# Kernel tuning notes

Measured on AMD Instinct MI355X. Metric: run time of the kernel, lower is better.

Reference implementation:

```python
import jax, jax.numpy as jnp
import numpy as np

EPS = 1e-6  # denominator guard used in LN Killing-ReLU


def ln_linear(W, x):
    # LNLinear: mix feature channels. x: [B,F,K,N], W: [G,F] -> [B,G,K,N]
    return jnp.einsum('gf,bfkn->bgkn', W, x)


def killing_so3(a, b):
    return -2.0 * jnp.sum(a * b, axis=2, keepdims=True)  # [B,F,1,N]


def ln_killing_relu(Wd, x):
    # LNKillingRelu: learned direction d, project out x's component along d
    # when the Killing form is non-negative (equivalent of VN-ReLU).
    d = ln_linear(Wd, x)
    kf = killing_so3(x, d)
    dd = killing_so3(d, d)
    return jnp.where(kf < 0, x, x - (kf / (dd + EPS)) * d)


def _forward(x, t, R, m, w1_lin, w1_dir, w2_lin, w2_dir, wb, wo):
    B = x.shape[0]
    x4 = x[..., None]  # [B,1,3,1]
    # control input u(t) = R @ 10*[sin t, cos t, sin t]
    u = R @ (10.0 * jnp.stack([jnp.sin(t), jnp.cos(t), jnp.sin(t)]))  # [3]
    u = jnp.broadcast_to(u[None, None, :, None], (B, 1, 3, 1))
    xin = jnp.concatenate([x4, u], axis=1)  # [B,2,3,1]

    # equivariant mixing matrices from learned m: [3,20] -> features [1,20,3,1]
    Rm = jnp.transpose(R @ m)[None, :, :, None]  # rearrange 'k f -> 1 f k 1'
    m1 = ln_killing_relu(w1_dir, ln_linear(w1_lin, Rm))  # [1,3,3,1]
    m2 = ln_killing_relu(w2_dir, ln_linear(w2_lin, Rm))
    m1 = jnp.transpose(m1[0, :, :, 0])  # rearrange '1 f k 1 -> k f' -> [3,3]
    m2 = jnp.transpose(m2[0, :, :, 0])
    M1 = m1 @ m1.T  # [3,3]
    M2 = m2 @ m2.T

    # LNLinearAndLieBracketChannelMix (residual_connect=True)
    h = ln_linear(wb, xin)  # [B,20,3,1]
    d1 = jnp.einsum('kl,bfln->bfkn', M1, h)
    d2 = jnp.einsum('kl,bfln->bfkn', M2, h)
    h = jnp.cross(d1, d2, axis=2) + h  # so3 Lie bracket = cross product; residual

    out = ln_linear(wo, h)  # [B,1,3,1]
    return out[..., 0]  # rearrange 'b f d 1 -> b f d'


def setup_inputs():
    key = jax.random.key(0)
    ks = jax.random.split(key, 8)
    B, FM = 1000000, 20
    x = jax.random.normal(ks[0], (B, 1, 3), dtype=jnp.float32)
    t = jnp.array(0.7, dtype=jnp.float32)
    R = jnp.eye(3, dtype=jnp.float32)
    m = 0.1 * jax.random.normal(ks[1], (3, FM), dtype=jnp.float32)
    w1_lin = jax.random.normal(ks[2], (3, FM), dtype=jnp.float32) / np.sqrt(FM)
    w1_dir = jax.random.normal(ks[3], (3, 3), dtype=jnp.float32) / np.sqrt(3.0)
    w2_lin = jax.random.normal(ks[4], (3, FM), dtype=jnp.float32) / np.sqrt(FM)
    w2_dir = jax.random.normal(ks[5], (3, 3), dtype=jnp.float32) / np.sqrt(3.0)
    wb = jax.random.normal(ks[6], (FM, 2), dtype=jnp.float32) / np.sqrt(2.0)
    wo = jax.random.normal(ks[7], (1, FM), dtype=jnp.float32) / np.sqrt(FM)
    return {"x": x, "t": t, "R": R, "m": m, "w1_lin": w1_lin, "w1_dir": w1_dir,
            "w2_lin": w2_lin, "w2_dir": w2_dir, "wb": wb, "wo": wo}


def reference(x, t, R, m, w1_lin, w1_dir, w2_lin, w2_dir, wb, wo):
    return _forward(x, t, R, m, w1_lin, w1_dir, w2_lin, w2_dir, wb, wo)
```

## Files before the change

### kernel.cpp

```cpp
#include <hip/hip_runtime.h>
#include <math.h>

#define LN_EPS 1e-6f


__device__ inline void compute_M(const float* wl , const float* wd ,
                                 const float Rm[20][3], float M[3][3]) {
    float y[3][3];
    for (int g = 0; g < 3; ++g)
        for (int k = 0; k < 3; ++k) {
            float s = 0.f;
            for (int f = 0; f < 20; ++f) s += wl[g * 20 + f] * Rm[f][k];
            y[g][k] = s;
        }
    float d[3][3];
    for (int g = 0; g < 3; ++g)
        for (int k = 0; k < 3; ++k) {
            float s = 0.f;
            for (int f = 0; f < 3; ++f) s += wd[g * 3 + f] * y[f][k];
            d[g][k] = s;
        }
    float mm[3][3];
    for (int f = 0; f < 3; ++f) {
        float kf = -2.f * (y[f][0] * d[f][0] + y[f][1] * d[f][1] + y[f][2] * d[f][2]);
        float dd = -2.f * (d[f][0] * d[f][0] + d[f][1] * d[f][1] + d[f][2] * d[f][2]);
        float coef = kf / (dd + LN_EPS);
        for (int k = 0; k < 3; ++k)
            mm[f][k] = (kf < 0.f) ? y[f][k] : (y[f][k] - coef * d[f][k]);
    }
    for (int k = 0; k < 3; ++k)
        for (int l = 0; l < 3; ++l) {
            float s = 0.f;
            for (int f = 0; f < 3; ++f) s += mm[f][k] * mm[f][l];
            M[k][l] = s;
        }
}

__global__ void setup_kernel(const float* __restrict__ t, const float* __restrict__ R,
                             const float* __restrict__ m, const float* __restrict__ w1l,
                             const float* __restrict__ w1d, const float* __restrict__ w2l,
                             const float* __restrict__ w2d, const float* __restrict__ wb,
                             const float* __restrict__ wo, float* __restrict__ ws) {
    if (threadIdx.x != 0 || blockIdx.x != 0) return;

    const float tt = t[0];
    const float st = sinf(tt), ct = cosf(tt);
    const float uv[3] = {10.f * st, 10.f * ct, 10.f * st};
    float u[3];
    for (int i = 0; i < 3; ++i)
        u[i] = R[i * 3 + 0] * uv[0] + R[i * 3 + 1] * uv[1] + R[i * 3 + 2] * uv[2];

    float Rm[20][3];
    for (int f = 0; f < 20; ++f)
        for (int k = 0; k < 3; ++k) {
            float s = 0.f;
            for (int j = 0; j < 3; ++j) s += R[k * 3 + j] * m[j * 20 + f];
            Rm[f][k] = s;
        }

    float M1[3][3], M2[3][3];
    compute_M(w1l, w1d, Rm, M1);
    compute_M(w2l, w2d, Rm, M2);

    float v1[3], v2[3];
    for (int k = 0; k < 3; ++k) {
        v1[k] = M1[k][0] * u[0] + M1[k][1] * u[1] + M1[k][2] * u[2];
        v2[k] = M2[k][0] * u[0] + M2[k][1] * u[1] + M2[k][2] * u[2];
    }

    float Sa = 0.f, Sb = 0.f, Saa = 0.f, Sab = 0.f, Sbb = 0.f;
    for (int g = 0; g < 20; ++g) {
        float a = wb[g * 2 + 0], b = wb[g * 2 + 1], w = wo[g];
        Sa += w * a; Sb += w * b;
        Saa += w * a * a; Sab += w * a * b; Sbb += w * b * b;
    }

    auto hat = [](const float v[3], float H[3][3]) {
        H[0][0] = 0.f;    H[0][1] = -v[2]; H[0][2] = v[1];
        H[1][0] = v[2];   H[1][1] = 0.f;   H[1][2] = -v[0];
        H[2][0] = -v[1];  H[2][1] = v[0];  H[2][2] = 0.f;
    };
    float H1[3][3], H2[3][3];
    hat(v1, H1);
    hat(v2, H2);

    float A[3][3];
    for (int i = 0; i < 3; ++i)
        for (int j = 0; j < 3; ++j) {
            float s = 0.f;
            for (int k = 0; k < 3; ++k)
                s += -H2[i][k] * M1[k][j] + H1[i][k] * M2[k][j];
            A[i][j] = Sab * s + ((i == j) ? Sa : 0.f);
        }

    float cr[3] = {v1[1] * v2[2] - v1[2] * v2[1],
                   v1[2] * v2[0] - v1[0] * v2[2],
                   v1[0] * v2[1] - v1[1] * v2[0]};
    float c0[3];
    for (int k = 0; k < 3; ++k) c0[k] = Sbb * cr[k] + Sb * u[k];

    for (int i = 0; i < 9; ++i) ws[i] = M1[i / 3][i % 3];
    for (int i = 0; i < 9; ++i) ws[9 + i] = M2[i / 3][i % 3];
    for (int i = 0; i < 9; ++i) ws[18 + i] = A[i / 3][i % 3];
    for (int k = 0; k < 3; ++k) ws[27 + k] = c0[k];
    ws[30] = Saa;
}


__device__ inline void point_op(const float* c, float X, float Y, float Z,
                                float& o0, float& o1, float& o2) {
    float p0 = c[0] * X + c[1] * Y + c[2] * Z;
    float p1 = c[3] * X + c[4] * Y + c[5] * Z;
    float p2 = c[6] * X + c[7] * Y + c[8] * Z;
    float q0 = c[9] * X + c[10] * Y + c[11] * Z;
    float q1 = c[12] * X + c[13] * Y + c[14] * Z;
    float q2 = c[15] * X + c[16] * Y + c[17] * Z;
    float cr0 = p1 * q2 - p2 * q1;
    float cr1 = p2 * q0 - p0 * q2;
    float cr2 = p0 * q1 - p1 * q0;
    float S = c[30];
    o0 = S * cr0 + c[18] * X + c[19] * Y + c[20] * Z + c[27];
    o1 = S * cr1 + c[21] * X + c[22] * Y + c[23] * Z + c[28];
    o2 = S * cr2 + c[24] * X + c[25] * Y + c[26] * Z + c[29];
}

__global__ __launch_bounds__(256) void main_kernel(const float* __restrict__ x,
                                                   float* __restrict__ out,
                                                   const float* __restrict__ ws,
                                                   int n4, int tail) {
    __shared__ float c[31];
    if (threadIdx.x < 31) c[threadIdx.x] = ws[threadIdx.x];
    __syncthreads();

    int tid = blockIdx.x * blockDim.x + threadIdx.x;

    if (tid < n4) {
        const float4* xin = (const float4*)x;
        float4 a = xin[tid * 3 + 0];
        float4 b = xin[tid * 3 + 1];
        float4 d = xin[tid * 3 + 2];
        float xs[12] = {a.x, a.y, a.z, a.w, b.x, b.y, b.z, b.w, d.x, d.y, d.z, d.w};
        float os[12];
#pragma unroll
        for (int p = 0; p < 4; ++p)
            point_op(c, xs[p * 3 + 0], xs[p * 3 + 1], xs[p * 3 + 2],
                     os[p * 3 + 0], os[p * 3 + 1], os[p * 3 + 2]);
        float4* op = (float4*)out;
        op[tid * 3 + 0] = make_float4(os[0], os[1], os[2], os[3]);
        op[tid * 3 + 1] = make_float4(os[4], os[5], os[6], os[7]);
        op[tid * 3 + 2] = make_float4(os[8], os[9], os[10], os[11]);
    } else if (tid == n4 && tail > 0) {
        for (int p = 0; p < tail; ++p) {
            int idx = n4 * 4 + p;
            float o0, o1, o2;
            point_op(c, x[idx * 3 + 0], x[idx * 3 + 1], x[idx * 3 + 2], o0, o1, o2);
            out[idx * 3 + 0] = o0;
            out[idx * 3 + 1] = o1;
            out[idx * 3 + 2] = o2;
        }
    }
}

extern "C" void kernel_launch(void* const* d_in, const int* in_sizes, int n_in,
                              void* d_out, int out_size, void* d_ws, size_t ws_size,
                              hipStream_t stream) {
    const float* x   = (const float*)d_in[0];
    const float* t   = (const float*)d_in[1];
    const float* R   = (const float*)d_in[2];
    const float* m   = (const float*)d_in[3];
    const float* w1l = (const float*)d_in[4];
    const float* w1d = (const float*)d_in[5];
    const float* w2l = (const float*)d_in[6];
    const float* w2d = (const float*)d_in[7];
    const float* wb  = (const float*)d_in[8];
    const float* wo  = (const float*)d_in[9];
    float* out = (float*)d_out;
    float* ws  = (float*)d_ws;

    const int B = in_sizes[0] / 3;
    const int n4 = B / 4;
    const int tail = B % 4;

    setup_kernel<<<1, 64, 0, stream>>>(t, R, m, w1l, w1d, w2l, w2d, wb, wo, ws);

    const int nthreads = n4 + (tail ? 1 : 0);
    const int blocks = (nthreads + 255) / 256;
    main_kernel<<<blocks, 256, 0, stream>>>(x, out, ws, n4, tail);
}
```

Before: 90.91 us.

## Fuse constant setup into main kernel and use nontemporal vector loads/stores

Removes the single-thread setup kernel and its workspace round trip. Every thread now recomputes the 31 derived constants from the small weight tensors, after issuing its nontemporal vector loads of x so that the redundant math overlaps the memory latency. This drops one kernel launch and the serial dependency between the two kernels. In exchange each thread does a few hundred extra FLOPs and uniform weight loads, and register pressure rises.

After: 92.01 us. Within noise of the previous version (+1.2%).

```diff
diff --git a/kernel.cpp b/kernel.cpp
--- a/kernel.cpp
+++ b/kernel.cpp
@@ -3,91 +3,103 @@
 
 #define LN_EPS 1e-6f
 
-
-__device__ inline void compute_M(const float* wl , const float* wd ,
-                                 const float Rm[20][3], float M[3][3]) {
+typedef float f32x4 __attribute__((ext_vector_type(4)));
+
+__device__ __forceinline__ void compute_M(const float* __restrict__ wl ,
+                                          const float* __restrict__ wd ,
+                                          const float Rm[20][3], float M[3][3]) {
     float y[3][3];
+#pragma unroll
     for (int g = 0; g < 3; ++g)
+#pragma unroll
         for (int k = 0; k < 3; ++k) {
             float s = 0.f;
+#pragma unroll
             for (int f = 0; f < 20; ++f) s += wl[g * 20 + f] * Rm[f][k];
             y[g][k] = s;
         }
     float d[3][3];
+#pragma unroll
     for (int g = 0; g < 3; ++g)
+#pragma unroll
         for (int k = 0; k < 3; ++k) {
             float s = 0.f;
+#pragma unroll
             for (int f = 0; f < 3; ++f) s += wd[g * 3 + f] * y[f][k];
             d[g][k] = s;
         }
     float mm[3][3];
+#pragma unroll
     for (int f = 0; f < 3; ++f) {
         float kf = -2.f * (y[f][0] * d[f][0] + y[f][1] * d[f][1] + y[f][2] * d[f][2]);
         float dd = -2.f * (d[f][0] * d[f][0] + d[f][1] * d[f][1] + d[f][2] * d[f][2]);
         float coef = kf / (dd + LN_EPS);
+#pragma unroll
         for (int k = 0; k < 3; ++k)
             mm[f][k] = (kf < 0.f) ? y[f][k] : (y[f][k] - coef * d[f][k]);
     }
+#pragma unroll
     for (int k = 0; k < 3; ++k)
+#pragma unroll
         for (int l = 0; l < 3; ++l) {
             float s = 0.f;
+#pragma unroll
             for (int f = 0; f < 3; ++f) s += mm[f][k] * mm[f][l];
             M[k][l] = s;
         }
 }
 
-__global__ void setup_kernel(const float* __restrict__ t, const float* __restrict__ R,
-                             const float* __restrict__ m, const float* __restrict__ w1l,
-                             const float* __restrict__ w1d, const float* __restrict__ w2l,
-                             const float* __restrict__ w2d, const float* __restrict__ wb,
-                             const float* __restrict__ wo, float* __restrict__ ws) {
-    if (threadIdx.x != 0 || blockIdx.x != 0) return;
-
+__device__ __forceinline__ void compute_constants(
+    const float* __restrict__ t, const float* __restrict__ R,
+    const float* __restrict__ m, const float* __restrict__ w1l,
+    const float* __restrict__ w1d, const float* __restrict__ w2l,
+    const float* __restrict__ w2d, const float* __restrict__ wb,
+    const float* __restrict__ wo, float c[31]) {
     const float tt = t[0];
     const float st = sinf(tt), ct = cosf(tt);
     const float uv[3] = {10.f * st, 10.f * ct, 10.f * st};
     float u[3];
+#pragma unroll
     for (int i = 0; i < 3; ++i)
         u[i] = R[i * 3 + 0] * uv[0] + R[i * 3 + 1] * uv[1] + R[i * 3 + 2] * uv[2];
 
     float Rm[20][3];
+#pragma unroll
     for (int f = 0; f < 20; ++f)
-        for (int k = 0; k < 3; ++k) {
-            float s = 0.f;
-            for (int j = 0; j < 3; ++j) s += R[k * 3 + j] * m[j * 20 + f];
-            Rm[f][k] = s;
-        }
+#pragma unroll
+        for (int k = 0; k < 3; ++k)
+            Rm[f][k] = R[k * 3 + 0] * m[0 * 20 + f] + R[k * 3 + 1] * m[1 * 20 + f] +
+                       R[k * 3 + 2] * m[2 * 20 + f];
 
     float M1[3][3], M2[3][3];
     compute_M(w1l, w1d, Rm, M1);
     compute_M(w2l, w2d, Rm, M2);
 
     float v1[3], v2[3];
+#pragma unroll
     for (int k = 0; k < 3; ++k) {
         v1[k] = M1[k][0] * u[0] + M1[k][1] * u[1] + M1[k][2] * u[2];
         v2[k] = M2[k][0] * u[0] + M2[k][1] * u[1] + M2[k][2] * u[2];
     }
 
     float Sa = 0.f, Sb = 0.f, Saa = 0.f, Sab = 0.f, Sbb = 0.f;
+#pragma unroll
     for (int g = 0; g < 20; ++g) {
         float a = wb[g * 2 + 0], b = wb[g * 2 + 1], w = wo[g];
         Sa += w * a; Sb += w * b;
         Saa += w * a * a; Sab += w * a * b; Sbb += w * b * b;
     }
 
-    auto hat = [](const float v[3], float H[3][3]) {
-        H[0][0] = 0.f;    H[0][1] = -v[2]; H[0][2] = v[1];
-        H[1][0] = v[2];   H[1][1] = 0.f;   H[1][2] = -v[0];
-        H[2][0] = -v[1];  H[2][1] = v[0];  H[2][2] = 0.f;
-    };
-    float H1[3][3], H2[3][3];
-    hat(v1, H1);
-    hat(v2, H2);
+    float H1[3][3] = {{0.f, -v1[2], v1[1]}, {v1[2], 0.f, -v1[0]}, {-v1[1], v1[0], 0.f}};
+    float H2[3][3] = {{0.f, -v2[2], v2[1]}, {v2[2], 0.f, -v2[0]}, {-v2[1], v2[0], 0.f}};
 
     float A[3][3];
+#pragma unroll
     for (int i = 0; i < 3; ++i)
+#pragma unroll
         for (int j = 0; j < 3; ++j) {
             float s = 0.f;
+#pragma unroll
             for (int k = 0; k < 3; ++k)
                 s += -H2[i][k] * M1[k][j] + H1[i][k] * M2[k][j];
             A[i][j] = Sab * s + ((i == j) ? Sa : 0.f);
@@ -96,19 +108,20 @@
     float cr[3] = {v1[1] * v2[2] - v1[2] * v2[1],
                    v1[2] * v2[0] - v1[0] * v2[2],
                    v1[0] * v2[1] - v1[1] * v2[0]};
-    float c0[3];
-    for (int k = 0; k < 3; ++k) c0[k] = Sbb * cr[k] + Sb * u[k];
-
-    for (int i = 0; i < 9; ++i) ws[i] = M1[i / 3][i % 3];
-    for (int i = 0; i < 9; ++i) ws[9 + i] = M2[i / 3][i % 3];
-    for (int i = 0; i < 9; ++i) ws[18 + i] = A[i / 3][i % 3];
-    for (int k = 0; k < 3; ++k) ws[27 + k] = c0[k];
-    ws[30] = Saa;
-}
-
-
-__device__ inline void point_op(const float* c, float X, float Y, float Z,
-                                float& o0, float& o1, float& o2) {
+
+#pragma unroll
+    for (int i = 0; i < 9; ++i) c[i] = M1[i / 3][i % 3];
+#pragma unroll
+    for (int i = 0; i < 9; ++i) c[9 + i] = M2[i / 3][i % 3];
+#pragma unroll
+    for (int i = 0; i < 9; ++i) c[18 + i] = A[i / 3][i % 3];
+#pragma unroll
+    for (int k = 0; k < 3; ++k) c[27 + k] = Sbb * cr[k] + Sb * u[k];
+    c[30] = Saa;
+}
+
+__device__ __forceinline__ void point_op(const float c[31], float X, float Y, float Z,
+                                         float& o0, float& o1, float& o2) {
     float p0 = c[0] * X + c[1] * Y + c[2] * Z;
     float p1 = c[3] * X + c[4] * Y + c[5] * Z;
     float p2 = c[6] * X + c[7] * Y + c[8] * Z;
@@ -124,31 +137,41 @@
     o2 = S * cr2 + c[24] * X + c[25] * Y + c[26] * Z + c[29];
 }
 
-__global__ __launch_bounds__(256) void main_kernel(const float* __restrict__ x,
-                                                   float* __restrict__ out,
-                                                   const float* __restrict__ ws,
-                                                   int n4, int tail) {
-    __shared__ float c[31];
-    if (threadIdx.x < 31) c[threadIdx.x] = ws[threadIdx.x];
-    __syncthreads();
-
-    int tid = blockIdx.x * blockDim.x + threadIdx.x;
-
-    if (tid < n4) {
-        const float4* xin = (const float4*)x;
-        float4 a = xin[tid * 3 + 0];
-        float4 b = xin[tid * 3 + 1];
-        float4 d = xin[tid * 3 + 2];
+__global__ __launch_bounds__(256) void fused_kernel(
+    const float* __restrict__ x, float* __restrict__ out,
+    const float* __restrict__ t, const float* __restrict__ R,
+    const float* __restrict__ m, const float* __restrict__ w1l,
+    const float* __restrict__ w1d, const float* __restrict__ w2l,
+    const float* __restrict__ w2d, const float* __restrict__ wb,
+    const float* __restrict__ wo, int n4, int tail) {
+    const int tid = blockIdx.x * blockDim.x + threadIdx.x;
+    const bool vec_lane = tid < n4;
+
+    f32x4 a = {0.f, 0.f, 0.f, 0.f}, b = a, d = a;
+    if (vec_lane) {
+        const f32x4* xin = (const f32x4*)x;
+        a = __builtin_nontemporal_load(&xin[tid * 3 + 0]);
+        b = __builtin_nontemporal_load(&xin[tid * 3 + 1]);
+        d = __builtin_nontemporal_load(&xin[tid * 3 + 2]);
+    }
+
+    float c[31];
+    compute_constants(t, R, m, w1l, w1d, w2l, w2d, wb, wo, c);
+
+    if (vec_lane) {
         float xs[12] = {a.x, a.y, a.z, a.w, b.x, b.y, b.z, b.w, d.x, d.y, d.z, d.w};
         float os[12];
 #pragma unroll
         for (int p = 0; p < 4; ++p)
             point_op(c, xs[p * 3 + 0], xs[p * 3 + 1], xs[p * 3 + 2],
                      os[p * 3 + 0], os[p * 3 + 1], os[p * 3 + 2]);
-        float4* op = (float4*)out;
-        op[tid * 3 + 0] = make_float4(os[0], os[1], os[2], os[3]);
-        op[tid * 3 + 1] = make_float4(os[4], os[5], os[6], os[7]);
-        op[tid * 3 + 2] = make_float4(os[8], os[9], os[10], os[11]);
+        f32x4* op = (f32x4*)out;
+        f32x4 o0 = {os[0], os[1], os[2], os[3]};
+        f32x4 o1 = {os[4], os[5], os[6], os[7]};
+        f32x4 o2 = {os[8], os[9], os[10], os[11]};
+        __builtin_nontemporal_store(o0, &op[tid * 3 + 0]);
+        __builtin_nontemporal_store(o1, &op[tid * 3 + 1]);
+        __builtin_nontemporal_store(o2, &op[tid * 3 + 2]);
     } else if (tid == n4 && tail > 0) {
         for (int p = 0; p < tail; ++p) {
             int idx = n4 * 4 + p;
@@ -175,15 +198,13 @@
     const float* wb  = (const float*)d_in[8];
     const float* wo  = (const float*)d_in[9];
     float* out = (float*)d_out;
-    float* ws  = (float*)d_ws;
 
     const int B = in_sizes[0] / 3;
     const int n4 = B / 4;
     const int tail = B % 4;
 
-    setup_kernel<<<1, 64, 0, stream>>>(t, R, m, w1l, w1d, w2l, w2d, wb, wo, ws);
-
     const int nthreads = n4 + (tail ? 1 : 0);
     const int blocks = (nthreads + 255) / 256;
-    main_kernel<<<blocks, 256, 0, stream>>>(x, out, ws, n4, tail);
-}
+    fused_kernel<<<blocks, 256, 0, stream>>>(x, out, t, R, m, w1l, w1d, w2l, w2d, wb, wo,
+                                             n4, tail);
+}
```
